# Kernel optimization log

Measured on AMD Instinct MI355X. Metric: run time of the kernel, lower is better.

Reference implementation:

```python
import jax, jax.numpy as jnp
import numpy as np

N = 50000        # nodes
E = 1_600_000    # edges (avg degree 32)
G = 512          # graphs in batch
H = 128          # hidden
C_IN = 3
C_MID = 64
C_OUT = 2
EPS = 1e-5


def setup_inputs() -> dict:
    key = jax.random.key(0)
    ks = jax.random.split(key, 16)
    inp = {
        "x": jax.random.normal(ks[0], (N, C_IN), dtype=jnp.float32),
        "edge_index": jax.random.randint(ks[1], (2, E), 0, N, dtype=jnp.int64),
        "batch": jnp.sort(jax.random.randint(ks[2], (N,), 0, G, dtype=jnp.int64)),
        # GCNConv weights (PyG: out = norm_agg(x @ W) + b)
        "W1": jax.random.normal(ks[3], (C_IN, H), dtype=jnp.float32) / np.sqrt(C_IN),
        "b1": jnp.zeros((H,), jnp.float32),
        "W2": jax.random.normal(ks[4], (H, H), dtype=jnp.float32) / np.sqrt(H),
        "b2": jnp.zeros((H,), jnp.float32),
        "W3": jax.random.normal(ks[5], (H, H), dtype=jnp.float32) / np.sqrt(H),
        "b3": jnp.zeros((H,), jnp.float32),
        # BatchNorm affine params (input_bn, bn1, bn2, bn3)
        "bn0_g": jnp.ones((C_IN,), jnp.float32), "bn0_b": jnp.zeros((C_IN,), jnp.float32),
        "bn1_g": jnp.ones((H,), jnp.float32), "bn1_b": jnp.zeros((H,), jnp.float32),
        "bn2_g": jnp.ones((H,), jnp.float32), "bn2_b": jnp.zeros((H,), jnp.float32),
        "bn3_g": jnp.ones((H,), jnp.float32), "bn3_b": jnp.zeros((H,), jnp.float32),
        # classifier MLP
        "Wc1": jax.random.normal(ks[6], (H, C_MID), dtype=jnp.float32) / np.sqrt(H),
        "bc1": jnp.zeros((C_MID,), jnp.float32),
        "Wc2": jax.random.normal(ks[7], (C_MID, C_OUT), dtype=jnp.float32) / np.sqrt(C_MID),
        "bc2": jnp.zeros((C_OUT,), jnp.float32),
    }
    return inp


def _batchnorm(h, g, b):
    # training-mode BN over node dim (biased variance, as torch uses for normalization)
    m = h.mean(axis=0)
    v = jnp.mean((h - m) ** 2, axis=0)
    return (h - m) * jax.lax.rsqrt(v + EPS) * g + b


def _gcn_conv(h, W, b, src, dst, deg_inv_sqrt, deg_inv):
    # PyG GCNConv: symmetric normalization with self-loops.
    hw = h @ W                                        # [N, out]
    coef = deg_inv_sqrt[src] * deg_inv_sqrt[dst]      # [E]
    msg = hw[src] * coef[:, None]                     # [E, out]
    agg = jax.ops.segment_sum(msg, dst, num_segments=N)
    agg = agg + hw * deg_inv[:, None]                 # self-loop term (norm = 1/deg)
    return agg + b


def reference(x, edge_index, batch, W1, b1, W2, b2, W3, b3,
              bn0_g, bn0_b, bn1_g, bn1_b, bn2_g, bn2_b, bn3_g, bn3_b,
              Wc1, bc1, Wc2, bc2):
    src, dst = edge_index[0], edge_index[1]
    # degree with self-loops (in-degree at dst + 1)
    deg = jax.ops.segment_sum(jnp.ones((E,), jnp.float32), dst, num_segments=N) + 1.0
    deg_inv_sqrt = jax.lax.rsqrt(deg)
    deg_inv = 1.0 / deg

    h = _batchnorm(x, bn0_g, bn0_b)
    h = _batchnorm(jax.nn.relu(_gcn_conv(h, W1, b1, src, dst, deg_inv_sqrt, deg_inv)), bn1_g, bn1_b)
    h = _batchnorm(jax.nn.relu(_gcn_conv(h, W2, b2, src, dst, deg_inv_sqrt, deg_inv)), bn2_g, bn2_b)
    h = _batchnorm(jax.nn.relu(_gcn_conv(h, W3, b3, src, dst, deg_inv_sqrt, deg_inv)), bn3_g, bn3_b)

    # global mean pool over graphs
    sums = jax.ops.segment_sum(h, batch, num_segments=G)            # [G, H]
    cnts = jax.ops.segment_sum(jnp.ones((N,), jnp.float32), batch, num_segments=G)
    pooled = sums / jnp.maximum(cnts, 1.0)[:, None]

    # classifier (dropout = identity in eval)
    z = jax.nn.relu(pooled @ Wc1 + bc1)
    return z @ Wc2 + bc2
```

## Files before the change

### kernel.cpp

```cpp
#include <hip/hip_runtime.h>

#define NEPS 1e-5f
#define PAD 96

__device__ inline unsigned int bfpack(float a, float b) {
  unsigned int ua = __float_as_uint(a), ub = __float_as_uint(b);
  ua += 0x7fff + ((ua >> 16) & 1);
  ub += 0x7fff + ((ub >> 16) & 1);
  return (ua >> 16) | (ub & 0xffff0000u);
}
__device__ inline float bflo(unsigned int u) { return __uint_as_float(u << 16); }
__device__ inline float bfhi(unsigned int u) { return __uint_as_float(u & 0xffff0000u); }

__global__ void k_build(const int* __restrict__ ei, int* __restrict__ cnt,
                        int* __restrict__ csrp, int E_) {
  int e = blockIdx.x * 256 + threadIdx.x;
  if (e >= E_) return;
  int s = ei[e], d = ei[E_ + e];
  int slot = atomicAdd(&cnt[d], 1);
  if (slot < PAD) csrp[d * PAD + slot] = s;
}

__global__ __launch_bounds__(256) void k_node(const int* __restrict__ cnt,
                                              const float* __restrict__ x,
                                              float* __restrict__ dis, float4* __restrict__ xp,
                                              float* __restrict__ stats, int N_) {
  int b = blockIdx.x, t = threadIdx.x;
  int i = b * 256 + t;
  float s1[3] = {0, 0, 0}, s2[3] = {0, 0, 0};
  if (i < N_) {
    float dg = (float)cnt[i] + 1.0f;
    float ds_ = rsqrtf(dg);
    dis[i] = ds_;
    float x0 = x[i * 3 + 0], x1 = x[i * 3 + 1], x2 = x[i * 3 + 2];
    float4 v; v.x = ds_ * x0; v.y = ds_ * x1; v.z = ds_ * x2; v.w = ds_;
    xp[i] = v;
    s1[0] = x0; s1[1] = x1; s1[2] = x2;
    s2[0] = x0 * x0; s2[1] = x1 * x1; s2[2] = x2 * x2;
  }
  #pragma unroll
  for (int c = 0; c < 3; c++) {
    for (int off = 32; off > 0; off >>= 1) {
      s1[c] += __shfl_down(s1[c], off);
      s2[c] += __shfl_down(s2[c], off);
    }
  }
  __shared__ float rs[4][8];
  int lane = t & 63, w = t >> 6;
  if (lane == 0) {
    rs[w][0] = s1[0]; rs[w][1] = s1[1]; rs[w][2] = s1[2]; rs[w][3] = 0.f;
    rs[w][4] = s2[0]; rs[w][5] = s2[1]; rs[w][6] = s2[2]; rs[w][7] = 0.f;
  }
  __syncthreads();
  if (t < 8 && t != 3 && t != 7) {
    float a = rs[0][t] + rs[1][t] + rs[2][t] + rs[3][t];
    atomicAdd(&stats[t], a);
  }
}

__global__ __launch_bounds__(256) void k_layer1(const float4* __restrict__ xp,
                                                const int* __restrict__ csrp,
                                                const int* __restrict__ cnt,
                                                const float* __restrict__ stats,
                                                const float* __restrict__ g0,
                                                const float* __restrict__ b0,
                                                const float* __restrict__ W1,
                                                const float* __restrict__ b1,
                                                float* __restrict__ y,
                                                float* __restrict__ Sp,
                                                int N_) {
  __shared__ float wl[5 * 128];
  int t = threadIdx.x;
  float a_[3], dd_[3];
  #pragma unroll
  for (int c = 0; c < 3; c++) {
    float m = stats[c] / N_;
    float v = stats[4 + c] / N_ - m * m;
    float sc = g0[c] * rsqrtf(v + NEPS);
    a_[c] = sc; dd_[c] = b0[c] - m * sc;
  }
  for (int i = t; i < 384; i += 256) wl[i] = a_[i >> 7] * W1[i];
  for (int i = t; i < 128; i += 256) {
    wl[384 + i] = fmaf(dd_[0], W1[i], fmaf(dd_[1], W1[128 + i], dd_[2] * W1[256 + i]));
    wl[512 + i] = b1[i];
  }
  __syncthreads();
  int lane = t & 63, w = t >> 6;
  int c0 = lane * 2;
  float2 w0 = *(const float2*)&wl[c0];
  float2 w1 = *(const float2*)&wl[128 + c0];
  float2 w2 = *(const float2*)&wl[256 + c0];
  float2 uu = *(const float2*)&wl[384 + c0];
  float2 bb = *(const float2*)&wl[512 + c0];
  int wid = blockIdx.x * 4 + w;
  int nw = gridDim.x * 4;
  float s1x = 0, s1y = 0, s2x = 0, s2y = 0;
  for (int n = wid; n < N_; n += nw) {
    int dg = min(cnt[n], PAD);
    int base = n * PAD;
    float a0 = 0, a1 = 0, a2 = 0, sd = 0;
    for (int chunk = 0; chunk < dg; chunk += 64) {
      int cc = min(64, dg - chunk);
      if (lane < cc) {
        float4 v = xp[csrp[base + chunk + lane]];
        a0 += v.x; a1 += v.y; a2 += v.z; sd += v.w;
      }
    }
    #pragma unroll
    for (int m = 1; m < 64; m <<= 1) {
      a0 += __shfl_xor(a0, m);
      a1 += __shfl_xor(a1, m);
      a2 += __shfl_xor(a2, m);
      sd += __shfl_xor(sd, m);
    }
    float4 xn = xp[n];
    float dn = xn.w;
    a0 += xn.x; a1 += xn.y; a2 += xn.z; sd += xn.w;
    float z0 = dn * a0, z1 = dn * a1, z2 = dn * a2, zw = dn * sd;
    float ox = fmaxf(fmaf(z0, w0.x, fmaf(z1, w1.x, fmaf(z2, w2.x, fmaf(zw, uu.x, bb.x)))), 0.f);
    float oy = fmaxf(fmaf(z0, w0.y, fmaf(z1, w1.y, fmaf(z2, w2.y, fmaf(zw, uu.y, bb.y)))), 0.f);
    s1x += ox; s1y += oy; s2x += ox * ox; s2y += oy * oy;
    float2 o; o.x = ox; o.y = oy;
    *(float2*)&y[(size_t)n * 128 + c0] = o;
  }
  __shared__ float rs[4][64][4];
  rs[w][lane][0] = s1x; rs[w][lane][1] = s1y;
  rs[w][lane][2] = s2x; rs[w][lane][3] = s2y;
  __syncthreads();
  int s = t >> 7, c = t & 127;
  int lsrc = c >> 1, sl = (s << 1) | (c & 1);
  float a = rs[0][lsrc][sl] + rs[1][lsrc][sl] + rs[2][lsrc][sl] + rs[3][lsrc][sl];
  float* basep = Sp + (blockIdx.x & 7) * 256;
  atomicAdd(&basep[s * 128 + c], a);
}

__global__ __launch_bounds__(256) void k_gemm(const float* __restrict__ y,
                                              const float* __restrict__ W,
                                              const float* __restrict__ Sp,
                                              const float* __restrict__ g_,
                                              const float* __restrict__ b_,
                                              const float* __restrict__ dis,
                                              unsigned short* __restrict__ hwb, int N_) {
  int t = threadIdx.x;
  if (blockIdx.x == 0 && t < 64) ((unsigned int*)&hwb[(size_t)N_ * 128])[t] = 0;
  __shared__ float scs[128], shs[128];
  __shared__ float yl[64][128];
  if (t < 128) {
    float m_s = 0, v_s = 0;
    #pragma unroll
    for (int p = 0; p < 8; p++) { m_s += Sp[p * 256 + t]; v_s += Sp[p * 256 + 128 + t]; }
    float m = m_s / N_;
    float v = v_s / N_ - m * m;
    float s = g_[t] * rsqrtf(v + NEPS);
    scs[t] = s; shs[t] = b_[t] - m * s;
  }
  __syncthreads();
  int base = blockIdx.x * 64;
  for (int i = t; i < 64 * 32; i += 256) {
    int r = i >> 5;
    int cq = (i & 31) * 4;
    int n = base + r;
    float4 o = {0, 0, 0, 0};
    if (n < N_) {
      float4 v = *(const float4*)&y[(size_t)n * 128 + cq];
      float4 sc4 = *(const float4*)&scs[cq];
      float4 sh4 = *(const float4*)&shs[cq];
      o.x = fmaf(v.x, sc4.x, sh4.x);
      o.y = fmaf(v.y, sc4.y, sh4.y);
      o.z = fmaf(v.z, sc4.z, sh4.z);
      o.w = fmaf(v.w, sc4.w, sh4.w);
    }
    *(float4*)&yl[r][cq] = o;
  }
  __syncthreads();
  int tn = t >> 5, tj = t & 31;
  float4 acc[8];
  #pragma unroll
  for (int r = 0; r < 8; r++) acc[r] = float4{0, 0, 0, 0};
  for (int kk = 0; kk < 128; kk++) {
    float4 wv = *(const float4*)&W[kk * 128 + tj * 4];
    #pragma unroll
    for (int r = 0; r < 8; r++) {
      float yv = yl[tn * 8 + r][kk];
      acc[r].x = fmaf(yv, wv.x, acc[r].x);
      acc[r].y = fmaf(yv, wv.y, acc[r].y);
      acc[r].z = fmaf(yv, wv.z, acc[r].z);
      acc[r].w = fmaf(yv, wv.w, acc[r].w);
    }
  }
  #pragma unroll
  for (int r = 0; r < 8; r++) {
    int n = base + tn * 8 + r;
    if (n < N_) {
      float dn = dis[n];
      uint2 o;
      o.x = bfpack(acc[r].x * dn, acc[r].y * dn);
      o.y = bfpack(acc[r].z * dn, acc[r].w * dn);
      *(uint2*)&hwb[(size_t)n * 128 + tj * 4] = o;
    }
  }
}

template <int FUSE_POOL>
__global__ __launch_bounds__(256) void k_gatherb(const unsigned short* __restrict__ hwb,
                                                 const int* __restrict__ csrp,
                                                 const int* __restrict__ cnt,
                                                 const float* __restrict__ dis,
                                                 const float* __restrict__ bL,
                                                 float* __restrict__ y,
                                                 float* __restrict__ Sp,
                                                 const int* __restrict__ batch,
                                                 float* __restrict__ pooled, int N_) {
  int t = threadIdx.x;
  int lane = t & 63, w = t >> 6;
  int g16 = lane >> 4, l16 = lane & 15;
  int c0 = l16 * 8 + g16 * 2;
  float2 bb = *(const float2*)&bL[c0];
  const uint4* hw4 = (const uint4*)hwb;
  int wid = blockIdx.x * 4 + w;
  int nw = gridDim.x * 4;
  float s1a = 0, s1b = 0, s2a = 0, s2b = 0;
  for (int n = wid; n < N_; n += nw) {
    int dg = min(cnt[n], PAD);
    int base = n * PAD;
    float acc[8] = {0, 0, 0, 0, 0, 0, 0, 0};
    for (int chunk = 0; chunk < dg; chunk += 64) {
      int cc = min(64, dg - chunk);
      int idx = (lane < cc) ? csrp[base + chunk + lane] : N_;
      int nit = (cc + 3) >> 2;
      #pragma unroll 8
      for (int i = 0; i < nit; i++) {
        int s_ = __shfl(idx, i * 4 + g16);
        uint4 v = hw4[(size_t)s_ * 16 + l16];
        acc[0] += bflo(v.x); acc[1] += bfhi(v.x);
        acc[2] += bflo(v.y); acc[3] += bfhi(v.y);
        acc[4] += bflo(v.z); acc[5] += bfhi(v.z);
        acc[6] += bflo(v.w); acc[7] += bfhi(v.w);
      }
    }
    float dn = dis[n];
    {
      uint4 v = hw4[(size_t)n * 16 + l16];
      float wc = (g16 == 0) ? 1.f : 0.f;
      acc[0] = fmaf(wc, bflo(v.x), acc[0]); acc[1] = fmaf(wc, bfhi(v.x), acc[1]);
      acc[2] = fmaf(wc, bflo(v.y), acc[2]); acc[3] = fmaf(wc, bfhi(v.y), acc[3]);
      acc[4] = fmaf(wc, bflo(v.z), acc[4]); acc[5] = fmaf(wc, bfhi(v.z), acc[5]);
      acc[6] = fmaf(wc, bflo(v.w), acc[6]); acc[7] = fmaf(wc, bfhi(v.w), acc[7]);
    }
    #pragma unroll
    for (int k = 0; k < 8; k++) {
      acc[k] += __shfl_xor(acc[k], 16);
      acc[k] += __shfl_xor(acc[k], 32);
    }
    float ta = (g16 & 1) ? acc[2] : acc[0];
    float tb = (g16 & 1) ? acc[6] : acc[4];
    float va = (g16 & 2) ? tb : ta;
    float tc = (g16 & 1) ? acc[3] : acc[1];
    float td = (g16 & 1) ? acc[7] : acc[5];
    float vb = (g16 & 2) ? td : tc;
    float ox = fmaxf(fmaf(va, dn, bb.x), 0.f);
    float oy = fmaxf(fmaf(vb, dn, bb.y), 0.f);
    s1a += ox; s1b += oy; s2a += ox * ox; s2b += oy * oy;
    if (FUSE_POOL) {
      int g = batch[n];
      atomicAdd(&pooled[g * 128 + c0], ox);
      atomicAdd(&pooled[g * 128 + c0 + 1], oy);
    } else {
      float2 o; o.x = ox; o.y = oy;
      *(float2*)&y[(size_t)n * 128 + c0] = o;
    }
  }
  __shared__ float rs[4][64][4];
  rs[w][lane][0] = s1a; rs[w][lane][1] = s1b;
  rs[w][lane][2] = s2a; rs[w][lane][3] = s2b;
  __syncthreads();
  int s = t >> 7, c = t & 127;
  int lsrc = (c >> 3) | (((c & 7) >> 1) << 4);
  int sl = (s << 1) | (c & 1);
  float a = rs[0][lsrc][sl] + rs[1][lsrc][sl] + rs[2][lsrc][sl] + rs[3][lsrc][sl];
  float* basep = Sp + (blockIdx.x & 7) * 256;
  atomicAdd(&basep[s * 128 + c], a);
}

__device__ inline int lb_dev(const int* b, int n, int v) {
  int lo = 0, hi = n;
  while (lo < hi) { int mid = (lo + hi) >> 1; if (b[mid] < v) lo = mid + 1; else hi = mid; }
  return lo;
}

__global__ void k_cls(const float* __restrict__ pooled, const int* __restrict__ batch,
                      const float* __restrict__ Sp,
                      const float* __restrict__ g_, const float* __restrict__ b_,
                      const float* __restrict__ Wc1, const float* __restrict__ bc1,
                      const float* __restrict__ Wc2, const float* __restrict__ bc2,
                      float* __restrict__ out, int N_, int G_) {
  __shared__ float p[128];
  __shared__ float z[64];
  __shared__ int s_lo, s_hi;
  int g = blockIdx.x, t = threadIdx.x;
  if (t == 0) s_lo = lb_dev(batch, N_, g);
  if (t == 1) s_hi = lb_dev(batch, N_, g + 1);
  __syncthreads();
  float inv = 1.f / fmaxf((float)(s_hi - s_lo), 1.f);
  for (int k = t; k < 128; k += 64) {
    float m_s = 0, v_s = 0;
    #pragma unroll
    for (int q = 0; q < 8; q++) { m_s += Sp[q * 256 + k]; v_s += Sp[q * 256 + 128 + k]; }
    float m = m_s / N_;
    float v = v_s / N_ - m * m;
    float s = g_[k] * rsqrtf(v + NEPS);
    float sh = b_[k] - m * s;
    p[k] = fmaf(pooled[g * 128 + k] * inv, s, sh);
  }
  __syncthreads();
  float acc = bc1[t];
  for (int k = 0; k < 128; k++) acc = fmaf(p[k], Wc1[k * 64 + t], acc);
  z[t] = fmaxf(acc, 0.f);
  __syncthreads();
  if (t < 2) {
    float o = bc2[t];
    for (int j = 0; j < 64; j++) o = fmaf(z[j], Wc2[j * 2 + t], o);
    out[g * 2 + t] = o;
  }
}

extern "C" void kernel_launch(void* const* d_in, const int* in_sizes, int n_in,
                              void* d_out, int out_size, void* d_ws, size_t ws_size,
                              hipStream_t stream) {
  const float* x    = (const float*)d_in[0];
  const int*   ei   = (const int*)d_in[1];
  const int*   batch= (const int*)d_in[2];
  const float* W1   = (const float*)d_in[3];
  const float* b1   = (const float*)d_in[4];
  const float* W2   = (const float*)d_in[5];
  const float* b2   = (const float*)d_in[6];
  const float* W3   = (const float*)d_in[7];
  const float* b3   = (const float*)d_in[8];
  const float* bn0g = (const float*)d_in[9];
  const float* bn0b = (const float*)d_in[10];
  const float* bn1g = (const float*)d_in[11];
  const float* bn1b = (const float*)d_in[12];
  const float* bn2g = (const float*)d_in[13];
  const float* bn2b = (const float*)d_in[14];
  const float* bn3g = (const float*)d_in[15];
  const float* bn3b = (const float*)d_in[16];
  const float* Wc1  = (const float*)d_in[17];
  const float* bc1  = (const float*)d_in[18];
  const float* Wc2  = (const float*)d_in[19];
  const float* bc2  = (const float*)d_in[20];

  const int N_ = in_sizes[2];
  const int E_ = in_sizes[1] / 2;
  const int G_ = out_size / 2;

  char* ws = (char*)d_ws;
  size_t off = 0;
  auto A = [&](size_t bytes) { size_t o = off; off = (off + bytes + 255) & ~(size_t)255; return o; };
  size_t o_cnt   = A((size_t)N_ * 4);
  size_t o_stats = A((size_t)(256 + 3 * 2048) * 4);
  size_t o_pool  = A((size_t)G_ * 128 * 4);
  size_t zero_end = off;
  size_t o_csrp  = A((size_t)N_ * PAD * 4);
  size_t o_dis   = A((size_t)N_ * 4);
  size_t o_xp    = A((size_t)N_ * 16);
  size_t o_bufB  = A((size_t)N_ * 128 * 4);
  size_t o_bufAh = A(((size_t)N_ + 1) * 128 * 2);
  (void)ws_size; (void)n_in;

  int*   cnt     = (int*)(ws + o_cnt);
  float* stats   = (float*)(ws + o_stats);
  float* Sp1     = stats + 256;
  float* Sp2     = stats + 256 + 2048;
  float* Sp3     = stats + 256 + 4096;
  float* pooled  = (float*)(ws + o_pool);
  int*   csrp    = (int*)(ws + o_csrp);
  float* dis     = (float*)(ws + o_dis);
  float4* xp     = (float4*)(ws + o_xp);
  float* bufB    = (float*)(ws + o_bufB);
  unsigned short* bufAh = (unsigned short*)(ws + o_bufAh);

  hipMemsetAsync(ws, 0, zero_end, stream);

  int nb_node = (N_ + 255) / 256;
  int nb_edge = (E_ + 255) / 256;

  k_build<<<nb_edge, 256, 0, stream>>>(ei, cnt, csrp, E_);
  k_node<<<nb_node, 256, 0, stream>>>(cnt, x, dis, xp, stats, N_);

  k_layer1<<<2048, 256, 0, stream>>>(xp, csrp, cnt, stats, bn0g, bn0b, W1, b1, bufB, Sp1, N_);

  k_gemm<<<(N_ + 63) / 64, 256, 0, stream>>>(bufB, W2, Sp1, bn1g, bn1b, dis, bufAh, N_);
  k_gatherb<0><<<2048, 256, 0, stream>>>(bufAh, csrp, cnt, dis, b2, bufB, Sp2,
                                         batch, pooled, N_);

  k_gemm<<<(N_ + 63) / 64, 256, 0, stream>>>(bufB, W3, Sp2, bn2g, bn2b, dis, bufAh, N_);
  k_gatherb<1><<<2048, 256, 0, stream>>>(bufAh, csrp, cnt, dis, b3, nullptr, Sp3,
                                         batch, pooled, N_);

  k_cls<<<G_, 64, 0, stream>>>(pooled, batch, Sp3, bn3g, bn3b, Wc1, bc1, Wc2, bc2,
                               (float*)d_out, N_, G_);
}
```

Baseline: 358.9 us.

## Build compact CSR via two-level counting sort with 16-bit source indices

```diff
diff --git a/kernel.cpp b/kernel.cpp
--- a/kernel.cpp
+++ b/kernel.cpp
@@ -1,7 +1,6 @@
 #include <hip/hip_runtime.h>
 
 #define NEPS 1e-5f
-#define PAD 96
 
 __device__ inline unsigned int bfpack(float a, float b) {
   unsigned int ua = __float_as_uint(a), ub = __float_as_uint(b);
@@ -12,40 +11,119 @@
 __device__ inline float bflo(unsigned int u) { return __uint_as_float(u << 16); }
 __device__ inline float bfhi(unsigned int u) { return __uint_as_float(u & 0xffff0000u); }
 
-__global__ void k_build(const int* __restrict__ ei, int* __restrict__ cnt,
-                        int* __restrict__ csrp, int E_) {
-  int e = blockIdx.x * 256 + threadIdx.x;
-  if (e >= E_) return;
-  int s = ei[e], d = ei[E_ + e];
-  int slot = atomicAdd(&cnt[d], 1);
-  if (slot < PAD) csrp[d * PAD + slot] = s;
-}
-
-__global__ __launch_bounds__(256) void k_node(const int* __restrict__ cnt,
-                                              const float* __restrict__ x,
-                                              float* __restrict__ dis, float4* __restrict__ xp,
-                                              float* __restrict__ stats, int N_) {
-  int b = blockIdx.x, t = threadIdx.x;
-  int i = b * 256 + t;
+__device__ inline int blockScan256(int v, int t, int* tmp) {
+  int lane = t & 63, w = t >> 6;
+  #pragma unroll
+  for (int off = 1; off < 64; off <<= 1) {
+    int u = __shfl_up(v, off);
+    if (lane >= off) v += u;
+  }
+  if (lane == 63) tmp[w] = v;
+  __syncthreads();
+  int add = 0;
+  for (int k = 0; k < w; k++) add += tmp[k];
+  return v + add;
+}
+
+__global__ __launch_bounds__(256) void k_hist(const int* __restrict__ ei,
+                                              int* __restrict__ gh_pad, int E_) {
+  __shared__ int h[256];
+  int t = threadIdx.x;
+  h[t] = 0;
+  __syncthreads();
+  int i = blockIdx.x * 256 + t;
+  int stride = gridDim.x * 256;
+  for (int e = i; e < E_; e += stride) atomicAdd(&h[ei[E_ + e] >> 8], 1);
+  __syncthreads();
+  int c = h[t];
+  if (c) atomicAdd(&gh_pad[t * 16], c);
+}
+
+__global__ __launch_bounds__(256) void k_scan2(const int* __restrict__ gh_pad,
+                                               int* __restrict__ b_base,
+                                               int* __restrict__ cur_pad, int E_) {
+  __shared__ int tmp[4];
+  int t = threadIdx.x;
+  int c = gh_pad[t * 16];
+  int incl = blockScan256(c, t, tmp);
+  int excl = incl - c;
+  b_base[t] = excl;
+  cur_pad[t * 16] = excl;
+  if (t == 255) b_base[256] = incl;
+}
+
+__global__ __launch_bounds__(256) void k_part(const int* __restrict__ ei,
+                                              int* __restrict__ cur_pad,
+                                              unsigned int* __restrict__ kp, int E_) {
+  __shared__ int lh[256], lbase[256];
+  int t = threadIdx.x;
+  int start = blockIdx.x * 8192;
+  int end = min(start + 8192, E_);
+  lh[t] = 0;
+  __syncthreads();
+  for (int e = start + t; e < end; e += 256) atomicAdd(&lh[ei[E_ + e] >> 8], 1);
+  __syncthreads();
+  int c = lh[t];
+  if (c) lbase[t] = atomicAdd(&cur_pad[t * 16], c);
+  __syncthreads();
+  lh[t] = 0;
+  __syncthreads();
+  for (int e = start + t; e < end; e += 256) {
+    int d = ei[E_ + e], s = ei[e];
+    int bin = d >> 8;
+    int slot = atomicAdd(&lh[bin], 1);
+    kp[lbase[bin] + slot] = ((unsigned int)d << 16) | (unsigned int)s;
+  }
+}
+
+__global__ __launch_bounds__(256) void k_bucket(const unsigned int* __restrict__ kp,
+                                                const int* __restrict__ b_base,
+                                                unsigned short* __restrict__ csr16,
+                                                int* __restrict__ row_ptr, int* __restrict__ cnt,
+                                                const float* __restrict__ x,
+                                                float* __restrict__ dis, float4* __restrict__ xp,
+                                                float* __restrict__ stats, int N_) {
+  __shared__ int cur[256], offL[256], tmp[4];
+  __shared__ float rs[4][8];
+  int t = threadIdx.x, b = blockIdx.x;
+  int seg0 = b_base[b], seg1 = b_base[b + 1];
+  cur[t] = 0;
+  __syncthreads();
+  for (int e = seg0 + t; e < seg1; e += 256) atomicAdd(&cur[(kp[e] >> 16) & 255], 1);
+  __syncthreads();
+  int c = cur[t];
+  int incl = blockScan256(c, t, tmp);
+  offL[t] = incl - c;
+  __syncthreads();
+  cur[t] = 0;
+  __syncthreads();
+  for (int e = seg0 + t; e < seg1; e += 256) {
+    unsigned int v = kp[e];
+    int dl = (v >> 16) & 255;
+    int slot = atomicAdd(&cur[dl], 1);
+    csr16[seg0 + offL[dl] + slot] = (unsigned short)(v & 0xffffu);
+  }
+  int n = b * 256 + t;
   float s1[3] = {0, 0, 0}, s2[3] = {0, 0, 0};
-  if (i < N_) {
-    float dg = (float)cnt[i] + 1.0f;
+  if (n < N_) {
+    row_ptr[n] = seg0 + offL[t];
+    cnt[n] = c;
+    float dg = (float)c + 1.0f;
     float ds_ = rsqrtf(dg);
-    dis[i] = ds_;
-    float x0 = x[i * 3 + 0], x1 = x[i * 3 + 1], x2 = x[i * 3 + 2];
+    dis[n] = ds_;
+    float x0 = x[n * 3 + 0], x1 = x[n * 3 + 1], x2 = x[n * 3 + 2];
     float4 v; v.x = ds_ * x0; v.y = ds_ * x1; v.z = ds_ * x2; v.w = ds_;
-    xp[i] = v;
+    xp[n] = v;
     s1[0] = x0; s1[1] = x1; s1[2] = x2;
     s2[0] = x0 * x0; s2[1] = x1 * x1; s2[2] = x2 * x2;
   }
   #pragma unroll
-  for (int c = 0; c < 3; c++) {
+  for (int cc = 0; cc < 3; cc++) {
     for (int off = 32; off > 0; off >>= 1) {
-      s1[c] += __shfl_down(s1[c], off);
-      s2[c] += __shfl_down(s2[c], off);
-    }
-  }
-  __shared__ float rs[4][8];
+      s1[cc] += __shfl_down(s1[cc], off);
+      s2[cc] += __shfl_down(s2[cc], off);
+    }
+  }
   int lane = t & 63, w = t >> 6;
   if (lane == 0) {
     rs[w][0] = s1[0]; rs[w][1] = s1[1]; rs[w][2] = s1[2]; rs[w][3] = 0.f;
@@ -59,7 +137,8 @@
 }
 
 __global__ __launch_bounds__(256) void k_layer1(const float4* __restrict__ xp,
-                                                const int* __restrict__ csrp,
+                                                const unsigned short* __restrict__ csr16,
+                                                const int* __restrict__ row_ptr,
                                                 const int* __restrict__ cnt,
                                                 const float* __restrict__ stats,
                                                 const float* __restrict__ g0,
@@ -96,13 +175,13 @@
   int nw = gridDim.x * 4;
   float s1x = 0, s1y = 0, s2x = 0, s2y = 0;
   for (int n = wid; n < N_; n += nw) {
-    int dg = min(cnt[n], PAD);
-    int base = n * PAD;
+    int dg = cnt[n];
+    int base = row_ptr[n];
     float a0 = 0, a1 = 0, a2 = 0, sd = 0;
     for (int chunk = 0; chunk < dg; chunk += 64) {
       int cc = min(64, dg - chunk);
       if (lane < cc) {
-        float4 v = xp[csrp[base + chunk + lane]];
+        float4 v = xp[csr16[base + chunk + lane]];
         a0 += v.x; a1 += v.y; a2 += v.z; sd += v.w;
       }
     }
@@ -203,7 +282,8 @@
 
 template <int FUSE_POOL>
 __global__ __launch_bounds__(256) void k_gatherb(const unsigned short* __restrict__ hwb,
-                                                 const int* __restrict__ csrp,
+                                                 const unsigned short* __restrict__ csr16,
+                                                 const int* __restrict__ row_ptr,
                                                  const int* __restrict__ cnt,
                                                  const float* __restrict__ dis,
                                                  const float* __restrict__ bL,
@@ -221,12 +301,12 @@
   int nw = gridDim.x * 4;
   float s1a = 0, s1b = 0, s2a = 0, s2b = 0;
   for (int n = wid; n < N_; n += nw) {
-    int dg = min(cnt[n], PAD);
-    int base = n * PAD;
+    int dg = cnt[n];
+    int base = row_ptr[n];
     float acc[8] = {0, 0, 0, 0, 0, 0, 0, 0};
     for (int chunk = 0; chunk < dg; chunk += 64) {
       int cc = min(64, dg - chunk);
-      int idx = (lane < cc) ? csrp[base + chunk + lane] : N_;
+      int idx = (lane < cc) ? (int)csr16[base + chunk + lane] : N_;
       int nit = (cc + 3) >> 2;
       #pragma unroll 8
       for (int i = 0; i < nit; i++) {
@@ -352,28 +432,39 @@
   const int N_ = in_sizes[2];
   const int E_ = in_sizes[1] / 2;
   const int G_ = out_size / 2;
+  const int NB = (N_ + 255) / 256;
 
   char* ws = (char*)d_ws;
   size_t off = 0;
   auto A = [&](size_t bytes) { size_t o = off; off = (off + bytes + 255) & ~(size_t)255; return o; };
-  size_t o_cnt   = A((size_t)N_ * 4);
+  size_t o_gh    = A(256 * 16 * 4);
   size_t o_stats = A((size_t)(256 + 3 * 2048) * 4);
   size_t o_pool  = A((size_t)G_ * 128 * 4);
   size_t zero_end = off;
-  size_t o_csrp  = A((size_t)N_ * PAD * 4);
+  size_t o_cur   = A(256 * 16 * 4);
+  size_t o_bbase = A(257 * 4);
+  size_t o_kp    = A((size_t)E_ * 4);
+  size_t o_csr16 = A(((size_t)E_ + 64) * 2);
+  size_t o_rowp  = A((size_t)N_ * 4);
+  size_t o_cnt   = A((size_t)N_ * 4);
   size_t o_dis   = A((size_t)N_ * 4);
   size_t o_xp    = A((size_t)N_ * 16);
   size_t o_bufB  = A((size_t)N_ * 128 * 4);
   size_t o_bufAh = A(((size_t)N_ + 1) * 128 * 2);
   (void)ws_size; (void)n_in;
 
-  int*   cnt     = (int*)(ws + o_cnt);
+  int*   gh_pad  = (int*)(ws + o_gh);
   float* stats   = (float*)(ws + o_stats);
   float* Sp1     = stats + 256;
   float* Sp2     = stats + 256 + 2048;
   float* Sp3     = stats + 256 + 4096;
   float* pooled  = (float*)(ws + o_pool);
-  int*   csrp    = (int*)(ws + o_csrp);
+  int*   cur_pad = (int*)(ws + o_cur);
+  int*   b_base  = (int*)(ws + o_bbase);
+  unsigned int* kp = (unsigned int*)(ws + o_kp);
+  unsigned short* csr16 = (unsigned short*)(ws + o_csr16);
+  int*   row_ptr = (int*)(ws + o_rowp);
+  int*   cnt     = (int*)(ws + o_cnt);
   float* dis     = (float*)(ws + o_dis);
   float4* xp     = (float4*)(ws + o_xp);
   float* bufB    = (float*)(ws + o_bufB);
@@ -381,20 +472,20 @@
 
   hipMemsetAsync(ws, 0, zero_end, stream);
 
-  int nb_node = (N_ + 255) / 256;
-  int nb_edge = (E_ + 255) / 256;
-
-  k_build<<<nb_edge, 256, 0, stream>>>(ei, cnt, csrp, E_);
-  k_node<<<nb_node, 256, 0, stream>>>(cnt, x, dis, xp, stats, N_);
-
-  k_layer1<<<2048, 256, 0, stream>>>(xp, csrp, cnt, stats, bn0g, bn0b, W1, b1, bufB, Sp1, N_);
+  k_hist<<<256, 256, 0, stream>>>(ei, gh_pad, E_);
+  k_scan2<<<1, 256, 0, stream>>>(gh_pad, b_base, cur_pad, E_);
+  k_part<<<(E_ + 8191) / 8192, 256, 0, stream>>>(ei, cur_pad, kp, E_);
+  k_bucket<<<NB, 256, 0, stream>>>(kp, b_base, csr16, row_ptr, cnt, x, dis, xp, stats, N_);
+
+  k_layer1<<<2048, 256, 0, stream>>>(xp, csr16, row_ptr, cnt, stats, bn0g, bn0b, W1, b1,
+                                     bufB, Sp1, N_);
 
   k_gemm<<<(N_ + 63) / 64, 256, 0, stream>>>(bufB, W2, Sp1, bn1g, bn1b, dis, bufAh, N_);
-  k_gatherb<0><<<2048, 256, 0, stream>>>(bufAh, csrp, cnt, dis, b2, bufB, Sp2,
+  k_gatherb<0><<<2048, 256, 0, stream>>>(bufAh, csr16, row_ptr, cnt, dis, b2, bufB, Sp2,
                                          batch, pooled, N_);
 
   k_gemm<<<(N_ + 63) / 64, 256, 0, stream>>>(bufB, W3, Sp2, bn2g, bn2b, dis, bufAh, N_);
-  k_gatherb<1><<<2048, 256, 0, stream>>>(bufAh, csrp, cnt, dis, b3, nullptr, Sp3,
+  k_gatherb<1><<<2048, 256, 0, stream>>>(bufAh, csr16, row_ptr, cnt, dis, b3, nullptr, Sp3,
                                          batch, pooled, N_);
 
   k_cls<<<G_, 64, 0, stream>>>(pooled, batch, Sp3, bn3g, bn3b, Wc1, bc1, Wc2, bc2,
```

Result: faster. 296.1 us (-17.5%).
